# Performance work log

Hardware: AMD Instinct MI355X
Metric: run time of the kernel (lower is better)

## Reference

```python
import jax, jax.numpy as jnp
import numpy as np

BLANK_ID = 0
B, MAX_T, MAX_U, VOCAB = 4, 200, 101, 1024  # MAX_U = max_label_len + 1


def setup_inputs() -> dict:
    key = jax.random.key(0)
    k1, k2, k3 = jax.random.split(key, 3)
    logits = jax.random.normal(k1, (B, MAX_T, MAX_U, VOCAB), dtype=jnp.float32)
    labels = jax.random.randint(k2, (B, MAX_U - 1), 0, VOCAB).astype(jnp.int64)
    label_lengths = jax.random.randint(k3, (B,), 1, MAX_U).astype(jnp.int64)  # in [1, MAX_U-1]
    attention_mask = jnp.ones((B, MAX_T), dtype=jnp.int32)
    return {"logits": logits, "labels": labels,
            "label_lengths": label_lengths, "attention_mask": attention_mask}


def _alpha_lattice(blank_lp, label_lp):
    """Forward variables for one sample.

    blank_lp: [T, U]   log P(blank | t, u)
    label_lp: [T, U-1] log P(y_u | t, u)  (label emitted at grid column u)
    Returns alpha [T, U], matching the reference recursion:
      alpha[0,0]   = blank_lp[0,0]
      alpha[t,0]   = alpha[t-1,0] + blank_lp[t,0]
      alpha[0,u]   = alpha[0,u-1] + label_lp[0,u-1]
      alpha[t,u]   = logaddexp(alpha[t-1,u]+blank_lp[t,u], alpha[t,u-1]+label_lp[t,u-1])
    """
    # First row: pure label path (cumulative sum along u).
    row0 = blank_lp[0, 0] + jnp.concatenate(
        [jnp.zeros((1,), blank_lp.dtype), jnp.cumsum(label_lp[0])])

    def time_step(prev_row, xs):
        b_t, l_t = xs                 # [U], [U-1]
        from_blank = prev_row + b_t   # blank transition into row t

        def u_step(carry, x):
            bl, lb = x
            a = jnp.logaddexp(bl, carry + lb)
            return a, a

        _, rest = jax.lax.scan(u_step, from_blank[0], (from_blank[1:], l_t))
        row = jnp.concatenate([from_blank[:1], rest])
        return row, row

    _, rows = jax.lax.scan(time_step, row0, (blank_lp[1:], label_lp[1:]))
    return jnp.concatenate([row0[None], rows], axis=0)  # [T, U]


def reference(logits, labels, label_lengths, attention_mask):
    Bn, maxT, maxU, V = logits.shape
    input_lengths = jnp.clip(attention_mask.sum(axis=1).astype(jnp.int32), 1, maxT)
    lab_lens = jnp.clip(label_lengths.astype(jnp.int32), 0, maxU - 1)
    labels_c = jnp.clip(labels, 0, V - 1)

    lp = jax.nn.log_softmax(logits, axis=-1)          # [B, T, U, V]
    blank_lp = lp[..., BLANK_ID]                      # [B, T, U]
    # label_lp[b, t, u] = lp[b, t, u, labels[b, u]] for u in [0, U-2]
    idx = jnp.broadcast_to(labels_c[:, None, :, None], (Bn, maxT, maxU - 1, 1))
    label_lp = jnp.take_along_axis(lp[:, :, :-1, :], idx, axis=3)[..., 0]

    alpha = jax.vmap(_alpha_lattice)(blank_lp, label_lp)  # [B, T, U]

    t_idx = input_lengths - 1
    u_idx = lab_lens                                  # U_b - 1 = label_len
    loss_b = -alpha[jnp.arange(Bn), t_idx, u_idx]

    valid = (input_lengths > 0) & (lab_lens > 0)
    loss_b = jnp.where(valid, loss_b, 0.0)
    num_valid = jnp.maximum(valid.sum(), 1)
    return loss_b.sum() / num_valid                   # reduction='mean'
```

## Files before the change

### kernel.cpp

```cpp
#include <hip/hip_runtime.h>
#include <hip/hip_bf16.h>
#include <math.h>

#define BB 4
#define TT 200
#define UU 101
#define VV 1024
#define NCELL (BB*TT*UU)

__device__ __forceinline__ float f4max(const float4& v) {
    return fmaxf(fmaxf(v.x, v.y), fmaxf(v.z, v.w));
}
__device__ __forceinline__ float f4comp(const float4& v, int c) {
    switch (c & 3) { case 0: return v.x; case 1: return v.y; case 2: return v.z; default: return v.w; }
}

__global__ __launch_bounds__(256) void lse_kernel(
        const float* __restrict__ logits,
        const int*   __restrict__ labels,
        float* __restrict__ blank_lp,
        float* __restrict__ label_lp) {
    const int wave = threadIdx.x >> 6;
    const int lane = threadIdx.x & 63;
    const int cell = blockIdx.x * 4 + wave;
    if (cell >= NCELL) return;
    const int b   = cell / (TT * UU);
    const int rem = cell % (TT * UU);
    const int t   = rem / UU;
    const int u   = rem % UU;

    const float4* src = (const float4*)(logits + (size_t)cell * VV);
    float4 x0 = src[lane];
    float4 x1 = src[lane + 64];
    float4 x2 = src[lane + 128];
    float4 x3 = src[lane + 192];

    float m = fmaxf(fmaxf(f4max(x0), f4max(x1)), fmaxf(f4max(x2), f4max(x3)));
    #pragma unroll
    for (int off = 32; off; off >>= 1) m = fmaxf(m, __shfl_xor(m, off));

    float s = 0.f;
    s += __expf(x0.x - m) + __expf(x0.y - m) + __expf(x0.z - m) + __expf(x0.w - m);
    s += __expf(x1.x - m) + __expf(x1.y - m) + __expf(x1.z - m) + __expf(x1.w - m);
    s += __expf(x2.x - m) + __expf(x2.y - m) + __expf(x2.z - m) + __expf(x2.w - m);
    s += __expf(x3.x - m) + __expf(x3.y - m) + __expf(x3.z - m) + __expf(x3.w - m);
    #pragma unroll
    for (int off = 32; off; off >>= 1) s += __shfl_xor(s, off);

    const float lse = m + __logf(s);

    if (lane == 0) blank_lp[cell] = x0.x - lse;

    if (u < UU - 1) {
        int l = labels[b * (UU - 1) + u];
        l = min(max(l, 0), VV - 1);
        const int lane_l = (l >> 2) & 63;
        if (lane == lane_l) {
            const int j = l >> 8;
            const int c = l & 3;
            float val = (j == 0) ? f4comp(x0, c) : (j == 1) ? f4comp(x1, c)
                      : (j == 2) ? f4comp(x2, c) : f4comp(x3, c);
            label_lp[(b * TT + t) * (UU - 1) + u] = val - lse;
        }
    }
}

__global__ __launch_bounds__(128) void alpha_kernel(
        const float* __restrict__ blank_lp,
        const float* __restrict__ label_lp,
        const int*   __restrict__ lab_lens,
        const int*   __restrict__ attn,
        float* __restrict__ loss_b,
        int*   __restrict__ valid_b) {
    const int b = blockIdx.x;
    const int u = threadIdx.x;

    __shared__ float buf[2][UU];
    __shared__ int   s_part[2];
    __shared__ float s_loss;

    int acc = 0;
    for (int i = threadIdx.x; i < TT; i += 128) acc += attn[b * TT + i];
    #pragma unroll
    for (int off = 32; off; off >>= 1) acc += __shfl_xor(acc, off);
    if ((threadIdx.x & 63) == 0) s_part[threadIdx.x >> 6] = acc;
    __syncthreads();
    int inlen = s_part[0] + s_part[1];
    inlen = min(max(inlen, 1), TT);
    const int tmax = inlen - 1;
    int lab = lab_lens[b];
    lab = min(max(lab, 0), UU - 1);
    const int ndiag = tmax + lab + 1;

    const float* bl_base = blank_lp + b * TT * UU;
    const float* lb_base = label_lp + b * TT * (UU - 1);
    const int um = min(u, UU - 1);
    const int ul = (um >= 1) ? (um - 1) : 0;

    auto fetch = [&](int d, float& fb, float& fl) {
        int tc = d - u;
        tc = min(max(tc, 0), TT - 1);
        fb = bl_base[tc * UU + um];
        fl = lb_base[tc * (UU - 1) + ul];
    };

    float cb[4], cl[4], nb[4], nl[4];
    #pragma unroll
    for (int k = 0; k < 4; ++k) fetch(k, cb[k], cl[k]);

    const int ng = (ndiag + 3) >> 2;
    for (int g = 0; g < ng; ++g) {
        const int dbase = g * 4;
        #pragma unroll
        for (int k = 0; k < 4; ++k) fetch(dbase + 4 + k, nb[k], nl[k]);
        #pragma unroll
        for (int k = 0; k < 4; ++k) {
            const int d = dbase + k;
            if (d < ndiag) {
                const int t = d - u;
                const bool act = (u <= lab) && (t >= 0) && (t <= tmax);
                if (act) {
                    const float fb = cb[k], fl = cl[k];
                    float v;
                    if (d == 0) {
                        v = fb;
                    } else if (u == 0) {
                        v = buf[(d - 1) & 1][0] + fb;
                    } else if (t == 0) {
                        v = buf[(d - 1) & 1][u - 1] + fl;
                    } else {
                        const float a = buf[(d - 1) & 1][u] + fb;
                        const float c = buf[(d - 1) & 1][u - 1] + fl;
                        const float mx = fmaxf(a, c), mn = fminf(a, c);
                        v = mx + log1pf(__expf(mn - mx));
                    }
                    buf[d & 1][u] = v;
                    if (t == tmax && u == lab) s_loss = -v;
                }
            }
            __syncthreads();
        }
        #pragma unroll
        for (int k = 0; k < 4; ++k) { cb[k] = nb[k]; cl[k] = nl[k]; }
    }

    if (threadIdx.x == 0) {
        loss_b[b]  = s_loss;
        valid_b[b] = (lab > 0) ? 1 : 0;
    }
}

__global__ void finalize_kernel(const float* __restrict__ loss_b,
                                const int* __restrict__ valid_b,
                                float* __restrict__ out) {
    if (threadIdx.x == 0 && blockIdx.x == 0) {
        float s = 0.f;
        int nv = 0;
        for (int b = 0; b < BB; ++b) {
            if (valid_b[b]) { s += loss_b[b]; ++nv; }
        }
        out[0] = s / (float)max(nv, 1);
    }
}

extern "C" void kernel_launch(void* const* d_in, const int* in_sizes, int n_in,
                              void* d_out, int out_size, void* d_ws, size_t ws_size,
                              hipStream_t stream) {
    const float* logits   = (const float*)d_in[0];
    const int*   labels   = (const int*)d_in[1];
    const int*   lab_lens = (const int*)d_in[2];
    const int*   attn     = (const int*)d_in[3];

    float* ws      = (float*)d_ws;
    float* blank   = ws;
    float* label   = blank + BB * TT * UU;
    float* loss_b  = label + BB * TT * (UU - 1);
    int*   valid_b = (int*)(loss_b + BB);

    lse_kernel<<<(NCELL + 3) / 4, 256, 0, stream>>>(logits, labels, blank, label);
    alpha_kernel<<<BB, 128, 0, stream>>>(blank, label, lab_lens, attn, loss_b, valid_b);
    finalize_kernel<<<1, 64, 0, stream>>>(loss_b, valid_b, (float*)d_out);
}
```

Baseline: 551.9 us.

## Store log-probs diagonal-major and run alpha recursion in a single wave

The softmax kernel now writes blank and label log-probs in a skewed diagonal-major layout, so each anti-diagonal of the lattice is one contiguous row. The alpha kernel uses a single 64-lane wave with two columns per lane and passes neighbour values through lane shuffles, replacing shared-memory double buffering and a block-wide barrier per diagonal. Loads become coalesced float2 reads with a small register prefetch queue. The skewed layout needs a larger workspace, and cells outside the valid lattice are never written, so the kernel relies on those entries never reaching the needed outputs.

```diff
diff --git a/kernel.cpp b/kernel.cpp
--- a/kernel.cpp
+++ b/kernel.cpp
@@ -7,6 +7,10 @@
 #define UU 101
 #define VV 1024
 #define NCELL (BB*TT*UU)
+
+#define DSTRIDE 102
+#define BROWS 300
+#define LROWS 301
 
 __device__ __forceinline__ float f4max(const float4& v) {
     return fmaxf(fmaxf(v.x, v.y), fmaxf(v.z, v.w));
@@ -18,8 +22,8 @@
 __global__ __launch_bounds__(256) void lse_kernel(
         const float* __restrict__ logits,
         const int*   __restrict__ labels,
-        float* __restrict__ blank_lp,
-        float* __restrict__ label_lp) {
+        float* __restrict__ blankD,
+        float* __restrict__ labD) {
     const int wave = threadIdx.x >> 6;
     const int lane = threadIdx.x & 63;
     const int cell = blockIdx.x * 4 + wave;
@@ -49,7 +53,8 @@
 
     const float lse = m + __logf(s);
 
-    if (lane == 0) blank_lp[cell] = x0.x - lse;
+    if (lane == 0)
+        blankD[(size_t)b * BROWS * DSTRIDE + (t + u) * DSTRIDE + u] = x0.x - lse;
 
     if (u < UU - 1) {
         int l = labels[b * (UU - 1) + u];
@@ -60,91 +65,96 @@
             const int c = l & 3;
             float val = (j == 0) ? f4comp(x0, c) : (j == 1) ? f4comp(x1, c)
                       : (j == 2) ? f4comp(x2, c) : f4comp(x3, c);
-            label_lp[(b * TT + t) * (UU - 1) + u] = val - lse;
+            labD[(size_t)b * LROWS * DSTRIDE + (t + u + 1) * DSTRIDE + (u + 1)] = val - lse;
         }
     }
 }
 
-__global__ __launch_bounds__(128) void alpha_kernel(
-        const float* __restrict__ blank_lp,
-        const float* __restrict__ label_lp,
+__global__ __launch_bounds__(64) void alpha_kernel(
+        const float* __restrict__ blankD,
+        const float* __restrict__ labD,
         const int*   __restrict__ lab_lens,
         const int*   __restrict__ attn,
         float* __restrict__ loss_b,
         int*   __restrict__ valid_b) {
     const int b = blockIdx.x;
-    const int u = threadIdx.x;
+    const int lane = threadIdx.x;
 
-    __shared__ float buf[2][UU];
-    __shared__ int   s_part[2];
     __shared__ float s_loss;
+    if (lane == 0) s_loss = 0.f;
 
     int acc = 0;
-    for (int i = threadIdx.x; i < TT; i += 128) acc += attn[b * TT + i];
+    for (int i = lane; i < TT; i += 64) acc += attn[b * TT + i];
     #pragma unroll
     for (int off = 32; off; off >>= 1) acc += __shfl_xor(acc, off);
-    if ((threadIdx.x & 63) == 0) s_part[threadIdx.x >> 6] = acc;
-    __syncthreads();
-    int inlen = s_part[0] + s_part[1];
-    inlen = min(max(inlen, 1), TT);
+    const int inlen = min(max(acc, 1), TT);
     const int tmax = inlen - 1;
     int lab = lab_lens[b];
     lab = min(max(lab, 0), UU - 1);
     const int ndiag = tmax + lab + 1;
 
-    const float* bl_base = blank_lp + b * TT * UU;
-    const float* lb_base = label_lp + b * TT * (UU - 1);
-    const int um = min(u, UU - 1);
-    const int ul = (um >= 1) ? (um - 1) : 0;
+    const float* blb = blankD + (size_t)b * BROWS * DSTRIDE;
+    const float* llb = labD   + (size_t)b * LROWS * DSTRIDE;
 
-    auto fetch = [&](int d, float& fb, float& fl) {
-        int tc = d - u;
-        tc = min(max(tc, 0), TT - 1);
-        fb = bl_base[tc * UU + um];
-        fl = lb_base[tc * (UU - 1) + ul];
+    const int c0 = 2 * lane;
+    const int c1 = 2 * lane + 1;
+    const int cc = min(c0, 100);
+
+    auto loadB = [&](int d) -> float2 {
+        return *(const float2*)(blb + min(d, BROWS - 1) * DSTRIDE + cc);
+    };
+    auto loadL = [&](int d) -> float2 {
+        return *(const float2*)(llb + min(d, LROWS - 1) * DSTRIDE + cc);
     };
 
-    float cb[4], cl[4], nb[4], nl[4];
+    constexpr int Q = 4;
+    float2 qb[Q], ql[Q];
     #pragma unroll
-    for (int k = 0; k < 4; ++k) fetch(k, cb[k], cl[k]);
+    for (int k = 0; k < Q; ++k) { qb[k] = loadB(k); ql[k] = loadL(k); }
 
-    const int ng = (ndiag + 3) >> 2;
-    for (int g = 0; g < ng; ++g) {
-        const int dbase = g * 4;
-        #pragma unroll
-        for (int k = 0; k < 4; ++k) fetch(dbase + 4 + k, nb[k], nl[k]);
-        #pragma unroll
-        for (int k = 0; k < 4; ++k) {
-            const int d = dbase + k;
-            if (d < ndiag) {
-                const int t = d - u;
-                const bool act = (u <= lab) && (t >= 0) && (t <= tmax);
-                if (act) {
-                    const float fb = cb[k], fl = cl[k];
-                    float v;
-                    if (d == 0) {
-                        v = fb;
-                    } else if (u == 0) {
-                        v = buf[(d - 1) & 1][0] + fb;
-                    } else if (t == 0) {
-                        v = buf[(d - 1) & 1][u - 1] + fl;
-                    } else {
-                        const float a = buf[(d - 1) & 1][u] + fb;
-                        const float c = buf[(d - 1) & 1][u - 1] + fl;
-                        const float mx = fmaxf(a, c), mn = fminf(a, c);
-                        v = mx + log1pf(__expf(mn - mx));
-                    }
-                    buf[d & 1][u] = v;
-                    if (t == tmax && u == lab) s_loss = -v;
-                }
-            }
-            __syncthreads();
+    float prevA = 0.f, prevB = 0.f;
+
+    for (int d = 0; d < ndiag; ++d) {
+        const int slot = d & (Q - 1);
+        const float2 bl = qb[slot];
+        const float2 lb = ql[slot];
+        qb[slot] = loadB(d + Q);
+        ql[slot] = loadL(d + Q);
+
+        const float upB = __shfl_up(prevB, 1);
+
+        float newA;
+        if (lane == 0) {
+            newA = (d == 0) ? bl.x : prevA + bl.x;
+        } else if (d == c0) {
+            newA = upB + lb.x;
+        } else {
+            const float a = prevA + bl.x;
+            const float c = upB + lb.x;
+            const float mx = fmaxf(a, c), mn = fminf(a, c);
+            newA = mx + __logf(1.f + __expf(mn - mx));
         }
-        #pragma unroll
-        for (int k = 0; k < 4; ++k) { cb[k] = nb[k]; cl[k] = nl[k]; }
+
+        float newB;
+        if (d == c1) {
+            newB = prevA + lb.y;
+        } else {
+            const float a = prevB + bl.y;
+            const float c = prevA + lb.y;
+            const float mx = fmaxf(a, c), mn = fminf(a, c);
+            newB = mx + __logf(1.f + __expf(mn - mx));
+        }
+
+        if (d == ndiag - 1) {
+            if (c0 == lab) s_loss = -newA;
+            if (c1 == lab) s_loss = -newB;
+        }
+        prevA = newA;
+        prevB = newB;
     }
 
-    if (threadIdx.x == 0) {
+    __syncthreads();
+    if (lane == 0) {
         loss_b[b]  = s_loss;
         valid_b[b] = (lab > 0) ? 1 : 0;
     }
@@ -172,12 +182,12 @@
     const int*   attn     = (const int*)d_in[3];
 
     float* ws      = (float*)d_ws;
-    float* blank   = ws;
-    float* label   = blank + BB * TT * UU;
-    float* loss_b  = label + BB * TT * (UU - 1);
+    float* blankD  = ws;
+    float* labD    = blankD + BB * BROWS * DSTRIDE;
+    float* loss_b  = labD   + BB * LROWS * DSTRIDE;
     int*   valid_b = (int*)(loss_b + BB);
 
-    lse_kernel<<<(NCELL + 3) / 4, 256, 0, stream>>>(logits, labels, blank, label);
-    alpha_kernel<<<BB, 128, 0, stream>>>(blank, label, lab_lens, attn, loss_b, valid_b);
+    lse_kernel<<<(NCELL + 3) / 4, 256, 0, stream>>>(logits, labels, blankD, labD);
+    alpha_kernel<<<BB, 64, 0, stream>>>(blankD, labD, lab_lens, attn, loss_b, valid_b);
     finalize_kernel<<<1, 64, 0, stream>>>(loss_b, valid_b, (float*)d_out);
 }
```

Result: slower. 577.9 us (+4.7%).
